# Kernel optimization log

Measured on AMD Instinct MI355X. Metric: run time of the kernel, lower is better.

Reference implementation:

```python
import jax, jax.numpy as jnp
import numpy as np

B, N, D, S = 64, 1024, 8, 16
SPARSE_PROB = 0.1


def setup_inputs() -> dict:
    key = jax.random.key(0)
    k_x, k_m, k_ws, k_bd, k_wd, k_bs = jax.random.split(key, 6)
    x = jax.random.normal(k_x, (B, N, D, S), dtype=jnp.float32)
    # conexao='esparsa': (rand < 0.1).float() buffer, exactly like _criar_matriz_conexao
    matriz_conexao = (jax.random.uniform(k_m, (N, N)) < SPARSE_PROB).astype(jnp.float32)
    # Stacked per-neuron parameters of NeuronioDendritico
    w_syn = jax.random.normal(k_ws, (N, D, S), dtype=jnp.float32) * 0.1   # synapse weights
    b_dend = jax.random.normal(k_bd, (N, D), dtype=jnp.float32) * 0.1     # dendrite bias
    w_dend = jax.random.normal(k_wd, (N, D), dtype=jnp.float32) * 0.1     # dendrite->soma weights
    b_soma = jax.random.normal(k_bs, (N,), dtype=jnp.float32) * 0.1       # soma bias
    return {"x": x, "matriz_conexao": matriz_conexao, "w_syn": w_syn,
            "b_dend": b_dend, "w_dend": w_dend, "b_soma": b_soma}


def reference(x, matriz_conexao, w_syn, b_dend, w_dend, b_soma):
    # Connectivity mixing across neurons (conexao != 'densa'):
    # torch.einsum('bids,oi->bods', x, matriz_conexao)
    xm = jnp.einsum('bids,oi->bods', x, matriz_conexao)  # [B, N, D, S]
    # Fused batched version of the Python loop over n_neurons:
    # each dendrite: tanh(sum_s w*x + b)
    dend = jnp.tanh(jnp.einsum('bnds,nds->bnd', xm, w_syn) + b_dend[None])  # [B, N, D]
    # soma: weighted sum of dendritic outputs + bias -> sigmoid spike
    soma = jnp.einsum('bnd,nd->bn', dend, w_dend) + b_soma[None]            # [B, N]
    spikes = jax.nn.sigmoid(soma)
    return spikes
```

## Files before the change

kernel.cpp:

```cpp
#include <hip/hip_runtime.h>
#include <hip/hip_bf16.h>

#define BB 64
#define NN 1024
#define DD 8
#define SS 16
#define DS 128

typedef __attribute__((ext_vector_type(8))) short short8;
typedef __attribute__((ext_vector_type(4))) float floatx4;

typedef __attribute__((address_space(1))) const unsigned int glds_src;
typedef __attribute__((address_space(3))) unsigned int glds_dst;

static __device__ __forceinline__ unsigned short f2bf(float f) {
    unsigned int u = __float_as_uint(f);
    unsigned int r = (u + 0x7FFFu + ((u >> 16) & 1u)) >> 16;
    return (unsigned short)r;
}

__global__ void convert_M(const float* __restrict__ M, unsigned short* __restrict__ Mb) {
    int i = (blockIdx.x * 256 + threadIdx.x) * 4;
    float4 v = *(const float4*)(M + i);
    unsigned int p0 = (unsigned int)f2bf(v.x) | ((unsigned int)f2bf(v.y) << 16);
    unsigned int p1 = (unsigned int)f2bf(v.z) | ((unsigned int)f2bf(v.w) << 16);
    *(uint2*)(Mb + i) = make_uint2(p0, p1);
}

__global__ void transpose_x(const float* __restrict__ x, unsigned short* __restrict__ xT) {
    __shared__ float tile[64 * 68];
    const int t  = threadIdx.x;
    const int b  = blockIdx.z;
    const int i0 = blockIdx.x * 64;
    const int c0 = blockIdx.y * 64;
    const float* xb = x + (size_t)b * (NN * DS);

#pragma unroll
    for (int jj = 0; jj < 4; ++jj) {
        int il = (t >> 4) + jj * 16;
        int cl = (t & 15) * 4;
        float4 v = *(const float4*)(xb + (size_t)(i0 + il) * DS + c0 + cl);
        *(float4*)(tile + il * 68 + cl) = v;
    }
    __syncthreads();
    int cr  = t >> 2;
    int iq  = (t & 3) * 16;
    int rot = (t & 3) * 2;
    unsigned int p[8];
#pragma unroll
    for (int j = 0; j < 8; ++j) {
        int jp = (j + rot) & 7;
        unsigned short lo = f2bf(tile[(iq + 2 * jp + 0) * 68 + cr]);
        unsigned short hi = f2bf(tile[(iq + 2 * jp + 1) * 68 + cr]);
        p[jp] = (unsigned int)lo | ((unsigned int)hi << 16);
    }
    unsigned short* dst = xT + (size_t)b * (NN * DS) + (size_t)(c0 + cr) * NN + i0 + iq;
    *(uint4*)(dst + 0) = make_uint4(p[0], p[1], p[2], p[3]);
    *(uint4*)(dst + 8) = make_uint4(p[4], p[5], p[6], p[7]);
}

__global__ __launch_bounds__(256, 2) void gemm_fused(
    const unsigned short* __restrict__ Mb,
    const unsigned short* __restrict__ xT,
    const float* __restrict__ w_syn,
    const float* __restrict__ b_dend,
    const float* __restrict__ w_dend,
    const float* __restrict__ b_soma,
    float* __restrict__ out)
{
    __shared__ __align__(16) char smem[128 * 129 * 4];
    unsigned short* As = (unsigned short*)smem;
    unsigned short* Bs = As + 128 * 64;
    float* Cs = (float*)smem;

    const int t      = threadIdx.x;
    const int b      = blockIdx.x;
    const int o_base = blockIdx.y * 128;

    const char* AgB = (const char*)(Mb + (size_t)o_base * NN);
    const char* BgB = (const char*)(xT + (size_t)b * (NN * DS));

    const int lane = t & 63;
    const int w    = t >> 6;
    const int wr   = (w >> 1) * 64;
    const int wc   = (w & 1) * 64;
    const int lm   = lane & 15;
    const int kq   = lane >> 4;

    const int lr = lane >> 3;
    const int lg = (lane & 7) ^ lr;
    int off[4];
#pragma unroll
    for (int j = 0; j < 4; ++j)
        off[j] = ((w * 4 + j) * 8 + lr) * (NN * 2) + lg * 16;

    floatx4 acc[4][4] = {};

    for (int kt = 0; kt < 16; ++kt) {
        const int kb = kt * 128;
        __syncthreads();
#pragma unroll
        for (int j = 0; j < 4; ++j) {
            __builtin_amdgcn_global_load_lds(
                (glds_src*)(AgB + off[j] + kb),
                (glds_dst*)((char*)As + (w * 4 + j) * 1024), 16, 0, 0);
            __builtin_amdgcn_global_load_lds(
                (glds_src*)(BgB + off[j] + kb),
                (glds_dst*)((char*)Bs + (w * 4 + j) * 1024), 16, 0, 0);
        }
        __syncthreads();
#pragma unroll
        for (int ks = 0; ks < 2; ++ks) {
            short8 af[4], bf[4];
            const int g = (((ks * 4 + kq) ^ (lm & 7)) * 8);
#pragma unroll
            for (int r = 0; r < 4; ++r)
                af[r] = *(const short8*)(As + (wr + r * 16 + lm) * 64 + g);
#pragma unroll
            for (int c = 0; c < 4; ++c)
                bf[c] = *(const short8*)(Bs + (wc + c * 16 + lm) * 64 + g);
#pragma unroll
            for (int r = 0; r < 4; ++r)
#pragma unroll
                for (int c = 0; c < 4; ++c)
                    acc[r][c] = __builtin_amdgcn_mfma_f32_16x16x32_bf16(af[r], bf[c], acc[r][c], 0, 0, 0);
        }
    }

    __syncthreads();
#pragma unroll
    for (int r = 0; r < 4; ++r) {
#pragma unroll
        for (int c = 0; c < 4; ++c) {
            int col  = wc + c * 16 + lm;
            int row0 = wr + r * 16 + kq * 4;
            Cs[(row0 + 0) * 129 + col] = acc[r][c][0];
            Cs[(row0 + 1) * 129 + col] = acc[r][c][1];
            Cs[(row0 + 2) * 129 + col] = acc[r][c][2];
            Cs[(row0 + 3) * 129 + col] = acc[r][c][3];
        }
    }
    __syncthreads();

    {
        const int o_l = t >> 1;
        const int dh  = (t & 1) * 4;
        const int o   = o_base + o_l;
        float part = 0.f;
#pragma unroll
        for (int dd = 0; dd < 4; ++dd) {
            int d = dh + dd;
            float pre = b_dend[o * DD + d];
            const float* wsn = w_syn + (size_t)o * DS + d * SS;
            const float* cr  = Cs + o_l * 129 + d * SS;
#pragma unroll
            for (int s = 0; s < SS; ++s) pre += cr[s] * wsn[s];
            part += tanhf(pre) * w_dend[o * DD + d];
        }
        part += __shfl_xor(part, 1);
        if ((t & 1) == 0) {
            float soma = part + b_soma[o];
            out[(size_t)b * NN + o] = 1.f / (1.f + __expf(-soma));
        }
    }
}

extern "C" void kernel_launch(void* const* d_in, const int* in_sizes, int n_in,
                              void* d_out, int out_size, void* d_ws, size_t ws_size,
                              hipStream_t stream) {
    const float* x      = (const float*)d_in[0];
    const float* M      = (const float*)d_in[1];
    const float* w_syn  = (const float*)d_in[2];
    const float* b_dend = (const float*)d_in[3];
    const float* w_dend = (const float*)d_in[4];
    const float* b_soma = (const float*)d_in[5];
    float* out = (float*)d_out;

    unsigned short* xT = (unsigned short*)d_ws;
    unsigned short* Mb = xT + (size_t)BB * NN * DS;

    convert_M  <<<dim3(NN * NN / (256 * 4)), 256, 0, stream>>>(M, Mb);
    transpose_x<<<dim3(NN / 64, DS / 64, BB), 256, 0, stream>>>(x, xT);
    gemm_fused <<<dim3(BB, NN / 128), 256, 0, stream>>>(Mb, xT, w_syn, b_dend, w_dend, b_soma, out);
}
```

Measured before the change: 110.7 us.

## Double-buffer GEMM LDS tiles and reduce epilogue in registers via shuffles

Splits the A/B LDS tiles into two buffers so the async global-to-LDS loads for the next K tile are issued before the MFMAs on the current tile, leaving one barrier per iteration instead of two. It also drops the staging of the 128x128 fp32 result tile in shared memory: the synapse dot-product is done directly on accumulator registers with cross-lane shuffle reductions, and a small LDS array combines the two dendrite halves. LDS use rises to about 64KB for the tiles, which may limit occupancy under launch_bounds(256,2), and the epilogue now issues many more shuffles and strided w_syn loads.

```diff
diff --git a/kernel.cpp b/kernel.cpp
--- a/kernel.cpp
+++ b/kernel.cpp
@@ -68,10 +68,9 @@
     const float* __restrict__ b_soma,
     float* __restrict__ out)
 {
-    __shared__ __align__(16) char smem[128 * 129 * 4];
-    unsigned short* As = (unsigned short*)smem;
-    unsigned short* Bs = As + 128 * 64;
-    float* Cs = (float*)smem;
+    __shared__ __align__(16) unsigned short As[2][128 * 64];
+    __shared__ __align__(16) unsigned short Bs[2][128 * 64];
+    __shared__ float ex[128 * 2];
 
     const int t      = threadIdx.x;
     const int b      = blockIdx.x;
@@ -89,79 +88,91 @@
 
     const int lr = lane >> 3;
     const int lg = (lane & 7) ^ lr;
-    int off[4];
+    int off[4], ldsb[4];
 #pragma unroll
-    for (int j = 0; j < 4; ++j)
-        off[j] = ((w * 4 + j) * 8 + lr) * (NN * 2) + lg * 16;
+    for (int j = 0; j < 4; ++j) {
+        off[j]  = ((w * 4 + j) * 8 + lr) * (NN * 2) + lg * 16;
+        ldsb[j] = (w * 4 + j) * 1024;
+    }
 
     floatx4 acc[4][4] = {};
 
+#pragma unroll
+    for (int j = 0; j < 4; ++j) {
+        __builtin_amdgcn_global_load_lds((glds_src*)(AgB + off[j]),
+                                         (glds_dst*)((char*)As[0] + ldsb[j]), 16, 0, 0);
+        __builtin_amdgcn_global_load_lds((glds_src*)(BgB + off[j]),
+                                         (glds_dst*)((char*)Bs[0] + ldsb[j]), 16, 0, 0);
+    }
+    __syncthreads();
+
     for (int kt = 0; kt < 16; ++kt) {
-        const int kb = kt * 128;
-        __syncthreads();
+        if (kt < 15) {
+            const int kb = (kt + 1) * 128;
+            const int nb = (kt + 1) & 1;
 #pragma unroll
-        for (int j = 0; j < 4; ++j) {
-            __builtin_amdgcn_global_load_lds(
-                (glds_src*)(AgB + off[j] + kb),
-                (glds_dst*)((char*)As + (w * 4 + j) * 1024), 16, 0, 0);
-            __builtin_amdgcn_global_load_lds(
-                (glds_src*)(BgB + off[j] + kb),
-                (glds_dst*)((char*)Bs + (w * 4 + j) * 1024), 16, 0, 0);
+            for (int j = 0; j < 4; ++j) {
+                __builtin_amdgcn_global_load_lds((glds_src*)(AgB + off[j] + kb),
+                                                 (glds_dst*)((char*)As[nb] + ldsb[j]), 16, 0, 0);
+                __builtin_amdgcn_global_load_lds((glds_src*)(BgB + off[j] + kb),
+                                                 (glds_dst*)((char*)Bs[nb] + ldsb[j]), 16, 0, 0);
+            }
         }
-        __syncthreads();
+        const unsigned short* Ac = As[kt & 1];
+        const unsigned short* Bc = Bs[kt & 1];
 #pragma unroll
         for (int ks = 0; ks < 2; ++ks) {
             short8 af[4], bf[4];
             const int g = (((ks * 4 + kq) ^ (lm & 7)) * 8);
 #pragma unroll
             for (int r = 0; r < 4; ++r)
-                af[r] = *(const short8*)(As + (wr + r * 16 + lm) * 64 + g);
+                af[r] = *(const short8*)(Ac + (wr + r * 16 + lm) * 64 + g);
 #pragma unroll
             for (int c = 0; c < 4; ++c)
-                bf[c] = *(const short8*)(Bs + (wc + c * 16 + lm) * 64 + g);
+                bf[c] = *(const short8*)(Bc + (wc + c * 16 + lm) * 64 + g);
 #pragma unroll
             for (int r = 0; r < 4; ++r)
 #pragma unroll
                 for (int c = 0; c < 4; ++c)
                     acc[r][c] = __builtin_amdgcn_mfma_f32_16x16x32_bf16(af[r], bf[c], acc[r][c], 0, 0, 0);
         }
+        __syncthreads();
     }
 
-    __syncthreads();
+    float keep[4];
 #pragma unroll
     for (int r = 0; r < 4; ++r) {
 #pragma unroll
-        for (int c = 0; c < 4; ++c) {
-            int col  = wc + c * 16 + lm;
-            int row0 = wr + r * 16 + kq * 4;
-            Cs[(row0 + 0) * 129 + col] = acc[r][c][0];
-            Cs[(row0 + 1) * 129 + col] = acc[r][c][1];
-            Cs[(row0 + 2) * 129 + col] = acc[r][c][2];
-            Cs[(row0 + 3) * 129 + col] = acc[r][c][3];
+        for (int rg = 0; rg < 4; ++rg) {
+            const int o = o_base + wr + r * 16 + kq * 4 + rg;
+#pragma unroll
+            for (int c = 0; c < 4; ++c) {
+                const int d = (w & 1) * 4 + c;
+                float p = acc[r][c][rg] * w_syn[o * DS + d * SS + lm];
+                p += __shfl_xor(p, 1);
+                p += __shfl_xor(p, 2);
+                p += __shfl_xor(p, 4);
+                p += __shfl_xor(p, 8);
+                if (lm == r * 4 + rg) keep[c] = p;
+            }
         }
     }
-    __syncthreads();
-
     {
-        const int o_l = t >> 1;
-        const int dh  = (t & 1) * 4;
-        const int o   = o_base + o_l;
+        const int o_loc = wr + (lm >> 2) * 16 + kq * 4 + (lm & 3);
+        const int o     = o_base + o_loc;
         float part = 0.f;
 #pragma unroll
-        for (int dd = 0; dd < 4; ++dd) {
-            int d = dh + dd;
-            float pre = b_dend[o * DD + d];
-            const float* wsn = w_syn + (size_t)o * DS + d * SS;
-            const float* cr  = Cs + o_l * 129 + d * SS;
-#pragma unroll
-            for (int s = 0; s < SS; ++s) pre += cr[s] * wsn[s];
+        for (int c = 0; c < 4; ++c) {
+            const int d = (w & 1) * 4 + c;
+            float pre = keep[c] + b_dend[o * DD + d];
             part += tanhf(pre) * w_dend[o * DD + d];
         }
-        part += __shfl_xor(part, 1);
-        if ((t & 1) == 0) {
-            float soma = part + b_soma[o];
-            out[(size_t)b * NN + o] = 1.f / (1.f + __expf(-soma));
-        }
+        ex[o_loc * 2 + (w & 1)] = part;
+    }
+    __syncthreads();
+    if (t < 128) {
+        float soma = ex[t * 2] + ex[t * 2 + 1] + b_soma[o_base + t];
+        out[(size_t)b * NN + o_base + t] = 1.f / (1.f + __expf(-soma));
     }
 }
 
```

After: 113.2 us. 1.02x slower.
